# Kernel tuning notes

Hardware: AMD Instinct MI355X
Metric: run time of the kernel (lower is better)

Reference implementation:

```python
import jax, jax.numpy as jnp
import numpy as np

BN_EPS = 1e-5
ATT_EPS = 1e-6


def _conv(x, w, groups=1):
    # x: [B,C,H,W], w: [O, C//groups, k, k], stride 1, SAME padding for odd k
    k = w.shape[-1]
    p = (k - 1) // 2
    return jax.lax.conv_general_dilated(
        x, w, window_strides=(1, 1), padding=[(p, p), (p, p)],
        dimension_numbers=('NCHW', 'OIHW', 'NCHW'), feature_group_count=groups)


def _bn(x, bnp):
    # bnp: [4, C] stacked (scale, bias, running_mean, running_var); eval-mode BN
    s, b, m, v = bnp[0], bnp[1], bnp[2], bnp[3]
    inv = s / jnp.sqrt(v + BN_EPS)
    return x * inv[None, :, None, None] + (b - m * inv)[None, :, None, None]


def _relu6(x):
    return jnp.clip(x, 0.0, 6.0)


def _ffn(x, fc1_w, fc1_bn, conv1_w, conv1_bn, conv2_w, conv2_bn, fc2_w, fc2_bn):
    # E_FFN: 1x1 ConvBNReLU6 -> dw5x5 ConvBNReLU6 & dw3x3 ConvBNReLU6 -> sum -> 1x1 ConvBN -> ReLU6
    C = x.shape[1]
    h = _relu6(_bn(_conv(x, fc1_w), fc1_bn))
    x1 = _relu6(_bn(_conv(h, conv1_w, groups=C), conv1_bn))
    x2 = _relu6(_bn(_conv(h, conv2_w, groups=C), conv2_bn))
    return _relu6(_bn(_conv(x1 + x2, fc2_w), fc2_bn))


def _bias(y, b):
    return y + b[None, :, None, None]


def setup_inputs() -> dict:
    key = jax.random.key(0)
    ks = jax.random.split(key, 16)
    C, M = 64, 8  # in_places, in_places // scale
    B, H, W = 4, 224, 224

    def w(k, shape, s=0.05):
        return (jax.random.normal(k, shape, dtype=jnp.float32) * s)

    def bn_params(k, c):
        k1, k2, k3, k4 = jax.random.split(k, 4)
        scale = 1.0 + 0.1 * jax.random.normal(k1, (c,), dtype=jnp.float32)
        bias = 0.1 * jax.random.normal(k2, (c,), dtype=jnp.float32)
        mean = 0.1 * jax.random.normal(k3, (c,), dtype=jnp.float32)
        var = 1.0 + 0.1 * jax.random.uniform(k4, (c,), dtype=jnp.float32)
        return jnp.stack([scale, bias, mean, var])  # [4, c]

    return {
        'x': jax.random.normal(ks[0], (B, C, H, W), dtype=jnp.float32),
        'gamma': jnp.full((1,), 0.5, dtype=jnp.float32),  # nonzero so attention branch matters
        'q_w': w(ks[1], (M, C, 1, 1)), 'q_b': w(ks[2], (M,)),
        'k_w': w(ks[3], (M, C, 1, 1)), 'k_b': w(ks[4], (M,)),
        'v_w': w(ks[5], (C, C, 1, 1)), 'v_b': w(ks[6], (C,)),
        'fc1_w': w(ks[7], (C, C, 1, 1)), 'fc1_bn': bn_params(ks[8], C),
        'conv1_w': w(ks[9], (C, 1, 5, 5)), 'conv1_bn': bn_params(ks[10], C),
        'conv2_w': w(ks[11], (C, 1, 3, 3)), 'conv2_bn': bn_params(ks[12], C),
        'fc2_w': w(ks[13], (C, C, 1, 1)), 'fc2_bn': bn_params(ks[14], C),
    }


def reference(x, gamma, q_w, q_b, k_w, k_b, v_w, v_b,
              fc1_w, fc1_bn, conv1_w, conv1_bn, conv2_w, conv2_bn, fc2_w, fc2_bn):
    B, C, H, W = x.shape
    N = H * W
    x_channel = _ffn(x, fc1_w, fc1_bn, conv1_w, conv1_bn, conv2_w, conv2_bn, fc2_w, fc2_bn)
    # softplus feature maps; Q,K: [B, m, N]
    Q = jax.nn.softplus(_bias(_conv(x, q_w), q_b).reshape(B, -1, N))
    K = jax.nn.softplus(_bias(_conv(x, k_w), k_b).reshape(B, -1, N))
    V = (_bias(_conv(x, v_w), v_b) + x_channel).reshape(B, C, N)
    Qt = jnp.swapaxes(Q, 1, 2)                              # [B, N, m]
    KV = jnp.einsum('bmn,bcn->bmc', K, V)                   # [B, m, C]
    norm = 1.0 / jnp.einsum('bnm,bm->bn', Qt, K.sum(-1) + ATT_EPS)  # [B, N]
    wv = jnp.einsum('bnm,bmc,bn->bcn', Qt, KV, norm).reshape(B, C, H, W)
    return x + gamma * wv
```

## Files before the change

### kernel.cpp

```cpp
#include <hip/hip_runtime.h>
#include <math.h>

#define B_ 4
#define C_ 64
#define M_ 8
#define H_ 224
#define W_ 224
#define N_ (H_*W_)
#define CN_ (C_*N_)
#define MN_ (M_*N_)
#define BCN_ (B_*CN_)
#define BMN_ (B_*MN_)

__device__ __forceinline__ float relu6f(float v){ return fminf(fmaxf(v,0.0f),6.0f); }
__device__ __forceinline__ float softplusf(float v){
  return v > 0.0f ? v + log1pf(expf(-v)) : log1pf(expf(v));
}

#define FMA4(A, W, X) { A.x = fmaf((W), (X).x, A.x); A.y = fmaf((W), (X).y, A.y); \
                        A.z = fmaf((W), (X).z, A.z); A.w = fmaf((W), (X).w, A.w); }

__global__ __launch_bounds__(256) void k_fc1k(const float* __restrict__ x,
                                              const float* __restrict__ w,
                                              const float* __restrict__ bn,
                                              const float* __restrict__ kw,
                                              const float* __restrict__ kb,
                                              float* __restrict__ h,
                                              float* __restrict__ Kq)
{
  __shared__ float xsl[2*1024];
  __shared__ float wl [2*512];
  __shared__ float kt [512];
  const int tid  = threadIdx.x;
  const int b    = blockIdx.x / 392;
  const int pg   = blockIdx.x % 392;
  const int pix0 = pg*128;
  const float* xb = x + (size_t)b*CN_ + pix0;

  for (int idx = tid; idx < 512; idx += 256) {
    const int c = idx >> 3, m = idx & 7;
    kt[idx] = kw[m*64 + c];
  }

  const int scp = tid >> 5;
  const int spx = (tid & 31) << 2;
  const int e0 = tid*2, e1 = tid*2+1;
  const int wc0 = e0 >> 6, wo0 = e0 & 63;
  const int wc1 = e1 >> 6, wo1 = e1 & 63;

  {
    const float4 xr = *(const float4*)(xb + (size_t)scp*N_ + spx);
    const float w0r = w[wo0*64 + wc0];
    const float w1r = w[wo1*64 + wc1];
    *(float4*)&xsl[scp*128 + spx] = xr;
    wl[e0] = w0r; wl[e1] = w1r;
  }
  __syncthreads();

  const int lane = tid & 63, wv_ = tid >> 6;
  const int och  = 2*wv_ + (lane >> 5);
  const int ocb  = och*8;
  const int px4  = (lane & 31) << 2;

  float4 ah[8];
  float4 ak = {0,0,0,0};
  #pragma unroll
  for (int i = 0; i < 8; ++i) ah[i] = make_float4(0.f,0.f,0.f,0.f);

  for (int ck = 0; ck < 8; ++ck) {
    const int cur = ck & 1, nxt = cur ^ 1;
    const float* xc = &xsl[cur*1024];
    const float* wc = &wl[cur*512];
    float4 xr; float w0r, w1r;
    if (ck < 7) {
      const int c0n = (ck+1)*8;
      xr  = *(const float4*)(xb + (size_t)(c0n + scp)*N_ + spx);
      w0r = w[wo0*64 + c0n + wc0];
      w1r = w[wo1*64 + c0n + wc1];
    }
    #pragma unroll
    for (int cp = 0; cp < 8; ++cp) {
      const float4 xv = *(const float4*)&xc[cp*128 + px4];
      const float4 w0 = *(const float4*)&wc[cp*64 + ocb];
      const float4 w1 = *(const float4*)&wc[cp*64 + ocb + 4];
      const float kvw = kt[(ck*8+cp)*8 + och];
      FMA4(ah[0], w0.x, xv); FMA4(ah[1], w0.y, xv);
      FMA4(ah[2], w0.z, xv); FMA4(ah[3], w0.w, xv);
      FMA4(ah[4], w1.x, xv); FMA4(ah[5], w1.y, xv);
      FMA4(ah[6], w1.z, xv); FMA4(ah[7], w1.w, xv);
      FMA4(ak, kvw, xv);
    }
    if (ck < 7) {
      *(float4*)&xsl[nxt*1024 + scp*128 + spx] = xr;
      wl[nxt*512 + e0] = w0r; wl[nxt*512 + e1] = w1r;
    }
    __syncthreads();
  }

  float* hb = h + (size_t)b*CN_ + pix0 + px4;
  #pragma unroll
  for (int o = 0; o < 8; ++o) {
    const int oc = ocb + o;
    const float inv  = bn[oc] / sqrtf(bn[192+oc] + 1e-5f);
    const float beta = bn[64+oc] - bn[128+oc]*inv;
    float4 o4;
    o4.x = relu6f(fmaf(ah[o].x, inv, beta));
    o4.y = relu6f(fmaf(ah[o].y, inv, beta));
    o4.z = relu6f(fmaf(ah[o].z, inv, beta));
    o4.w = relu6f(fmaf(ah[o].w, inv, beta));
    *(float4*)(hb + (size_t)oc*N_) = o4;
  }
  {
    const float kbm = kb[och];
    float4 q;
    q.x = softplusf(ak.x + kbm); q.y = softplusf(ak.y + kbm);
    q.z = softplusf(ak.z + kbm); q.w = softplusf(ak.w + kbm);
    *(float4*)(Kq + (size_t)b*MN_ + (size_t)och*N_ + pix0 + px4) = q;
  }
}

__global__ __launch_bounds__(256) void k_dw(const float* __restrict__ h,
                                            const float* __restrict__ w5,
                                            const float* __restrict__ w3,
                                            const float* __restrict__ bn1,
                                            const float* __restrict__ bn2,
                                            float* __restrict__ s)
{
  __shared__ float tile[36*37];
  const int tid = threadIdx.x;
  const int blk = blockIdx.x;
  const int t   = blk % 49;
  const int bc  = blk / 49;
  const int c   = bc & 63;
  const int tx0 = (t % 7) * 32;
  const int ty0 = (t / 7) * 32;
  const float* hb = h + (size_t)bc * N_;

  for (int idx = tid; idx < 1296; idx += 256) {
    const int ly = idx / 36, lx = idx - ly*36;
    const int gy = ty0 + ly - 2, gx = tx0 + lx - 2;
    float v = 0.0f;
    if (gy >= 0 && gy < H_ && gx >= 0 && gx < W_) v = hb[gy*W_ + gx];
    tile[ly*37 + lx] = v;
  }
  __syncthreads();

  float w5r[25], w3r[9];
  #pragma unroll
  for (int i = 0; i < 25; ++i) w5r[i] = w5[c*25 + i];
  #pragma unroll
  for (int i = 0; i < 9; ++i)  w3r[i] = w3[c*9 + i];
  const float inv1 = bn1[c] / sqrtf(bn1[192+c] + 1e-5f);
  const float bet1 = bn1[64+c] - bn1[128+c]*inv1;
  const float inv2 = bn2[c] / sqrtf(bn2[192+c] + 1e-5f);
  const float bet2 = bn2[64+c] - bn2[128+c]*inv2;

  const int ty  = tid >> 3;
  const int tx4 = (tid & 7) << 2;
  float a5[4] = {0,0,0,0}, a3[4] = {0,0,0,0};
  #pragma unroll
  for (int dy = 0; dy < 5; ++dy) {
    float r[8];
    #pragma unroll
    for (int i = 0; i < 8; ++i) r[i] = tile[(ty+dy)*37 + tx4 + i];
    #pragma unroll
    for (int dx = 0; dx < 5; ++dx) {
      const float wv = w5r[dy*5+dx];
      #pragma unroll
      for (int p = 0; p < 4; ++p) a5[p] = fmaf(wv, r[p+dx], a5[p]);
    }
    if (dy >= 1 && dy <= 3) {
      #pragma unroll
      for (int dx = 1; dx <= 3; ++dx) {
        const float wv = w3r[(dy-1)*3+(dx-1)];
        #pragma unroll
        for (int p = 0; p < 4; ++p) a3[p] = fmaf(wv, r[p+dx], a3[p]);
      }
    }
  }
  float* sb = s + (size_t)bc * N_ + (ty0+ty)*W_ + tx0 + tx4;
  float4 o4;
  o4.x = relu6f(fmaf(a5[0],inv1,bet1)) + relu6f(fmaf(a3[0],inv2,bet2));
  o4.y = relu6f(fmaf(a5[1],inv1,bet1)) + relu6f(fmaf(a3[1],inv2,bet2));
  o4.z = relu6f(fmaf(a5[2],inv1,bet1)) + relu6f(fmaf(a3[2],inv2,bet2));
  o4.w = relu6f(fmaf(a5[3],inv1,bet1)) + relu6f(fmaf(a3[3],inv2,bet2));
  *(float4*)sb = o4;
}

__global__ __launch_bounds__(256) void k_v(const float* __restrict__ x,
                                           const float* __restrict__ s,
                                           const float* __restrict__ vw,
                                           const float* __restrict__ vb,
                                           const float* __restrict__ fw,
                                           const float* __restrict__ fbn,
                                           float* __restrict__ V)
{
  __shared__ float xsl[2*1024];
  __shared__ float ssl[2*1024];
  __shared__ float wvl[2*512];
  __shared__ float wfl[2*512];
  const int tid  = threadIdx.x;
  const int b    = blockIdx.x / 392;
  const int pg   = blockIdx.x % 392;
  const int pix0 = pg*128;
  const float* xb = x + (size_t)b*CN_ + pix0;
  const float* sb = s + (size_t)b*CN_ + pix0;

  const int scp = tid >> 5;
  const int spx = (tid & 31) << 2;
  const int e0 = tid*2, e1 = tid*2+1;
  const int wc0 = e0 >> 6, wo0 = e0 & 63;
  const int wc1 = e1 >> 6, wo1 = e1 & 63;

  {
    const float4 xr = *(const float4*)(xb + (size_t)scp*N_ + spx);
    const float4 sr = *(const float4*)(sb + (size_t)scp*N_ + spx);
    const float a0 = vw[wo0*64 + wc0], a1 = vw[wo1*64 + wc1];
    const float f0 = fw[wo0*64 + wc0], f1 = fw[wo1*64 + wc1];
    *(float4*)&xsl[scp*128 + spx] = xr;
    *(float4*)&ssl[scp*128 + spx] = sr;
    wvl[e0] = a0; wvl[e1] = a1;
    wfl[e0] = f0; wfl[e1] = f1;
  }
  __syncthreads();

  const int lane = tid & 63, wv_ = tid >> 6;
  const int och  = 2*wv_ + (lane >> 5);
  const int ocb  = och*8;
  const int px4  = (lane & 31) << 2;

  float4 av[8], af[8];
  #pragma unroll
  for (int i = 0; i < 8; ++i) { av[i] = make_float4(0,0,0,0); af[i] = make_float4(0,0,0,0); }

  for (int ck = 0; ck < 8; ++ck) {
    const int cur = ck & 1, nxt = cur ^ 1;
    const float* xc = &xsl[cur*1024];
    const float* sc2 = &ssl[cur*1024];
    const float* wvc = &wvl[cur*512];
    const float* wfc = &wfl[cur*512];
    float4 xr, sr; float a0r, a1r, f0r, f1r;
    if (ck < 7) {
      const int c0n = (ck+1)*8;
      xr  = *(const float4*)(xb + (size_t)(c0n + scp)*N_ + spx);
      sr  = *(const float4*)(sb + (size_t)(c0n + scp)*N_ + spx);
      a0r = vw[wo0*64 + c0n + wc0]; a1r = vw[wo1*64 + c0n + wc1];
      f0r = fw[wo0*64 + c0n + wc0]; f1r = fw[wo1*64 + c0n + wc1];
    }
    #pragma unroll
    for (int cp = 0; cp < 8; ++cp) {
      const float4 xv = *(const float4*)&xc[cp*128 + px4];
      const float4 sv = *(const float4*)&sc2[cp*128 + px4];
      const float4 wa0 = *(const float4*)&wvc[cp*64 + ocb];
      const float4 wa1 = *(const float4*)&wvc[cp*64 + ocb + 4];
      const float4 wf0 = *(const float4*)&wfc[cp*64 + ocb];
      const float4 wf1 = *(const float4*)&wfc[cp*64 + ocb + 4];
      FMA4(av[0], wa0.x, xv); FMA4(av[1], wa0.y, xv);
      FMA4(av[2], wa0.z, xv); FMA4(av[3], wa0.w, xv);
      FMA4(av[4], wa1.x, xv); FMA4(av[5], wa1.y, xv);
      FMA4(av[6], wa1.z, xv); FMA4(av[7], wa1.w, xv);
      FMA4(af[0], wf0.x, sv); FMA4(af[1], wf0.y, sv);
      FMA4(af[2], wf0.z, sv); FMA4(af[3], wf0.w, sv);
      FMA4(af[4], wf1.x, sv); FMA4(af[5], wf1.y, sv);
      FMA4(af[6], wf1.z, sv); FMA4(af[7], wf1.w, sv);
    }
    if (ck < 7) {
      *(float4*)&xsl[nxt*1024 + scp*128 + spx] = xr;
      *(float4*)&ssl[nxt*1024 + scp*128 + spx] = sr;
      wvl[nxt*512 + e0] = a0r; wvl[nxt*512 + e1] = a1r;
      wfl[nxt*512 + e0] = f0r; wfl[nxt*512 + e1] = f1r;
    }
    __syncthreads();
  }

  float* Vb = V + (size_t)b*CN_ + pix0 + px4;
  #pragma unroll
  for (int o = 0; o < 8; ++o) {
    const int oc = ocb + o;
    const float inv  = fbn[oc] / sqrtf(fbn[192+oc] + 1e-5f);
    const float beta = fbn[64+oc] - fbn[128+oc]*inv;
    const float bias = vb[oc];
    float4 o4;
    o4.x = av[o].x + bias + relu6f(fmaf(af[o].x, inv, beta));
    o4.y = av[o].y + bias + relu6f(fmaf(af[o].y, inv, beta));
    o4.z = av[o].z + bias + relu6f(fmaf(af[o].z, inv, beta));
    o4.w = av[o].w + bias + relu6f(fmaf(af[o].w, inv, beta));
    *(float4*)(Vb + (size_t)oc*N_) = o4;
  }
}

__global__ __launch_bounds__(256) void k_kv(const float* __restrict__ V,
                                            const float* __restrict__ Kq,
                                            float* __restrict__ KV,
                                            float* __restrict__ Ksum)
{
  const int blk = blockIdx.x;
  const int b   = blk >> 7;
  const int rem = blk & 127;
  const int cg  = rem >> 4;
  const int ch  = rem & 15;
  const int tid = threadIdx.x;
  const int base = ch * 3136;
  const int end  = base + 3136;
  const float* Kb = Kq + (size_t)b*MN_;
  const float* Vb = V  + (size_t)b*CN_ + (size_t)(cg*8)*N_;

  float acc[64];
  #pragma unroll
  for (int i = 0; i < 64; ++i) acc[i] = 0.0f;
  float ks[8] = {0,0,0,0,0,0,0,0};

  for (int n4 = base + tid*4; n4 < end; n4 += 1024) {
    float4 kr[8];
    #pragma unroll
    for (int m2 = 0; m2 < 8; ++m2) kr[m2] = *(const float4*)(Kb + (size_t)m2*N_ + n4);
    #pragma unroll
    for (int m2 = 0; m2 < 8; ++m2)
      ks[m2] += (kr[m2].x + kr[m2].y) + (kr[m2].z + kr[m2].w);
    #pragma unroll
    for (int c8 = 0; c8 < 8; ++c8) {
      const float4 vv = *(const float4*)(Vb + (size_t)c8*N_ + n4);
      #pragma unroll
      for (int m2 = 0; m2 < 8; ++m2) {
        float t = acc[m2*8+c8];
        t = fmaf(kr[m2].x, vv.x, t);
        t = fmaf(kr[m2].y, vv.y, t);
        t = fmaf(kr[m2].z, vv.z, t);
        t = fmaf(kr[m2].w, vv.w, t);
        acc[m2*8+c8] = t;
      }
    }
  }
  const int lane = tid & 63;

  {
    int nv = 64;
    #pragma unroll
    for (int mask = 1; mask <= 32; mask <<= 1) {
      nv >>= 1;
      const bool hi = (lane & mask) != 0;
      #pragma unroll
      for (int i = 0; i < 32; ++i) {
        if (i < nv) {
          const float mine = hi ? acc[i] : acc[i+nv];
          const float th = __shfl_xor(mine, mask);
          acc[i] = (hi ? acc[i+nv] : acc[i]) + th;
        }
      }
    }
  }
  const int j = 32*(lane & 1) + 16*((lane >> 1) & 1) + 8*((lane >> 2) & 1)
              + 4*((lane >> 3) & 1) + 2*((lane >> 4) & 1) + ((lane >> 5) & 1);
  atomicAdd(&KV[b*512 + (j >> 3)*64 + cg*8 + (j & 7)], acc[0]);

  if (cg == 0) {
    float mk = 0.0f;
    #pragma unroll
    for (int jj = 0; jj < 8; ++jj) {
      float v = ks[jj];
      v += __shfl_xor(v, 1);
      v += __shfl_xor(v, 2);
      v += __shfl_xor(v, 4);
      v += __shfl_xor(v, 8);
      v += __shfl_xor(v, 16);
      v += __shfl_xor(v, 32);
      if (lane == jj) mk = v;
    }
    if (lane < 8) atomicAdd(&Ksum[b*8 + lane], mk);
  }
}

__global__ __launch_bounds__(256) void k_out(const float* __restrict__ x,
                                             const float* __restrict__ qw,
                                             const float* __restrict__ qb,
                                             const float* __restrict__ gamma,
                                             const float* __restrict__ KV,
                                             const float* __restrict__ Ksum,
                                             float* __restrict__ out)
{
  __shared__ __align__(16) float kvt[64*8];
  __shared__ __align__(16) float wqt[64*8];
  __shared__ float ksl[8];
  const int tid = threadIdx.x;
  const int b  = blockIdx.x / 196;
  const int pg = blockIdx.x % 196;
  const int pix0 = pg*256;
  const float* xb = x + (size_t)b*CN_ + pix0 + tid;

  for (int idx = tid; idx < 512; idx += 256) {
    const int m = idx >> 6, c = idx & 63;
    kvt[c*8 + m] = KV[b*512 + idx];
    wqt[c*8 + m] = qw[idx];
  }
  if (tid < 8) ksl[tid] = Ksum[b*8 + tid] + 1e-6f;
  __syncthreads();

  float xr[64];
  float q[8] = {0,0,0,0,0,0,0,0};
  #pragma unroll
  for (int c = 0; c < 64; ++c) {
    xr[c] = xb[(size_t)c*N_];
    const float4 w0 = *(const float4*)&wqt[c*8];
    const float4 w1 = *(const float4*)&wqt[c*8+4];
    q[0] = fmaf(w0.x, xr[c], q[0]);
    q[1] = fmaf(w0.y, xr[c], q[1]);
    q[2] = fmaf(w0.z, xr[c], q[2]);
    q[3] = fmaf(w0.w, xr[c], q[3]);
    q[4] = fmaf(w1.x, xr[c], q[4]);
    q[5] = fmaf(w1.y, xr[c], q[5]);
    q[6] = fmaf(w1.z, xr[c], q[6]);
    q[7] = fmaf(w1.w, xr[c], q[7]);
  }
  float den = 0.0f;
  #pragma unroll
  for (int m = 0; m < 8; ++m) {
    q[m] = softplusf(q[m] + qb[m]);
    den  = fmaf(q[m], ksl[m], den);
  }
  const float sc = gamma[0] / den;

  float* ob = out + (size_t)b*CN_ + pix0 + tid;
  #pragma unroll
  for (int c = 0; c < 64; ++c) {
    const float4 k0 = *(const float4*)&kvt[c*8];
    const float4 k1 = *(const float4*)&kvt[c*8+4];
    float wv;
    wv = q[0]*k0.x;
    wv = fmaf(q[1], k0.y, wv);
    wv = fmaf(q[2], k0.z, wv);
    wv = fmaf(q[3], k0.w, wv);
    wv = fmaf(q[4], k1.x, wv);
    wv = fmaf(q[5], k1.y, wv);
    wv = fmaf(q[6], k1.z, wv);
    wv = fmaf(q[7], k1.w, wv);
    ob[(size_t)c*N_] = fmaf(sc, wv, xr[c]);
  }
}

extern "C" void kernel_launch(void* const* d_in, const int* in_sizes, int n_in,
                              void* d_out, int out_size, void* d_ws, size_t ws_size,
                              hipStream_t stream) {
  const float* x      = (const float*)d_in[0];
  const float* gamma  = (const float*)d_in[1];
  const float* q_w    = (const float*)d_in[2];
  const float* q_b    = (const float*)d_in[3];
  const float* k_w    = (const float*)d_in[4];
  const float* k_b    = (const float*)d_in[5];
  const float* v_w    = (const float*)d_in[6];
  const float* v_b    = (const float*)d_in[7];
  const float* fc1_w  = (const float*)d_in[8];
  const float* fc1_bn = (const float*)d_in[9];
  const float* c1_w   = (const float*)d_in[10];
  const float* c1_bn  = (const float*)d_in[11];
  const float* c2_w   = (const float*)d_in[12];
  const float* c2_bn  = (const float*)d_in[13];
  const float* fc2_w  = (const float*)d_in[14];
  const float* fc2_bn = (const float*)d_in[15];
  float* outp = (float*)d_out;

  float* ws   = (float*)d_ws;
  float* bufA = ws;
  float* bufS = ws + (size_t)BCN_;
  float* bufK = ws + (size_t)2*BCN_;
  float* kv   = ws + (size_t)2*BCN_ + BMN_;
  float* ksum = kv + 2048;

  hipMemsetAsync(kv, 0, (2048 + 32)*sizeof(float), stream);

  k_fc1k<<<dim3(B_*392), dim3(256), 0, stream>>>(x, fc1_w, fc1_bn, k_w, k_b, bufA, bufK);
  k_dw  <<<dim3(B_*C_*49), dim3(256), 0, stream>>>(bufA, c1_w, c2_w, c1_bn, c2_bn, bufS);
  k_v   <<<dim3(B_*392), dim3(256), 0, stream>>>(x, bufS, v_w, v_b, fc2_w, fc2_bn, bufA);
  k_kv  <<<dim3(512), dim3(256), 0, stream>>>(bufA, bufK, kv, ksum);
  k_out <<<dim3(B_*196), dim3(256), 0, stream>>>(x, q_w, q_b, gamma, kv, ksum, outp);
}
```

Before: 347.6 us.

## Compute softplus Q projection inside k_v and read it back in k_out

The 1x1 Q projection and its softplus move into k_v, which already has x staged in shared memory. The result is written into the FFN scratch buffer, which is no longer needed once the block has consumed it. k_out now loads the 8 precomputed Q channels instead of holding 64 channels of x in registers, and re-reads x only for the residual add. This removes k_out's large register array and its Q matmul, which should help occupancy. The cost is extra global writes and reads of the Q buffer.

```diff
diff --git a/kernel.cpp b/kernel.cpp
--- a/kernel.cpp
+++ b/kernel.cpp
@@ -188,23 +188,31 @@
 }
 
 __global__ __launch_bounds__(256) void k_v(const float* __restrict__ x,
-                                           const float* __restrict__ s,
+                                           float* __restrict__ s,
                                            const float* __restrict__ vw,
                                            const float* __restrict__ vb,
                                            const float* __restrict__ fw,
                                            const float* __restrict__ fbn,
+                                           const float* __restrict__ qw_,
+                                           const float* __restrict__ qb_,
                                            float* __restrict__ V)
 {
   __shared__ float xsl[2*1024];
   __shared__ float ssl[2*1024];
   __shared__ float wvl[2*512];
   __shared__ float wfl[2*512];
+  __shared__ float qt [512];
   const int tid  = threadIdx.x;
   const int b    = blockIdx.x / 392;
   const int pg   = blockIdx.x % 392;
   const int pix0 = pg*128;
   const float* xb = x + (size_t)b*CN_ + pix0;
   const float* sb = s + (size_t)b*CN_ + pix0;
+
+  for (int idx = tid; idx < 512; idx += 256) {
+    const int c = idx >> 3, m = idx & 7;
+    qt[idx] = qw_[m*64 + c];
+  }
 
   const int scp = tid >> 5;
   const int spx = (tid & 31) << 2;
@@ -230,6 +238,7 @@
   const int px4  = (lane & 31) << 2;
 
   float4 av[8], af[8];
+  float4 aq = {0,0,0,0};
   #pragma unroll
   for (int i = 0; i < 8; ++i) { av[i] = make_float4(0,0,0,0); af[i] = make_float4(0,0,0,0); }
 
@@ -255,6 +264,7 @@
       const float4 wa1 = *(const float4*)&wvc[cp*64 + ocb + 4];
       const float4 wf0 = *(const float4*)&wfc[cp*64 + ocb];
       const float4 wf1 = *(const float4*)&wfc[cp*64 + ocb + 4];
+      const float qvw = qt[(ck*8+cp)*8 + och];
       FMA4(av[0], wa0.x, xv); FMA4(av[1], wa0.y, xv);
       FMA4(av[2], wa0.z, xv); FMA4(av[3], wa0.w, xv);
       FMA4(av[4], wa1.x, xv); FMA4(av[5], wa1.y, xv);
@@ -263,6 +273,7 @@
       FMA4(af[2], wf0.z, sv); FMA4(af[3], wf0.w, sv);
       FMA4(af[4], wf1.x, sv); FMA4(af[5], wf1.y, sv);
       FMA4(af[6], wf1.z, sv); FMA4(af[7], wf1.w, sv);
+      FMA4(aq, qvw, xv);
     }
     if (ck < 7) {
       *(float4*)&xsl[nxt*1024 + scp*128 + spx] = xr;
@@ -286,6 +297,13 @@
     o4.z = av[o].z + bias + relu6f(fmaf(af[o].z, inv, beta));
     o4.w = av[o].w + bias + relu6f(fmaf(af[o].w, inv, beta));
     *(float4*)(Vb + (size_t)oc*N_) = o4;
+  }
+  {
+    const float qbm = qb_[och];
+    float4 q;
+    q.x = softplusf(aq.x + qbm); q.y = softplusf(aq.y + qbm);
+    q.z = softplusf(aq.z + qbm); q.w = softplusf(aq.w + qbm);
+    *(float4*)(s + (size_t)b*CN_ + (size_t)och*N_ + pix0 + px4) = q;
   }
 }
 
@@ -371,56 +389,38 @@
 }
 
 __global__ __launch_bounds__(256) void k_out(const float* __restrict__ x,
-                                             const float* __restrict__ qw,
-                                             const float* __restrict__ qb,
+                                             const float* __restrict__ Qbuf,
                                              const float* __restrict__ gamma,
                                              const float* __restrict__ KV,
                                              const float* __restrict__ Ksum,
                                              float* __restrict__ out)
 {
   __shared__ __align__(16) float kvt[64*8];
-  __shared__ __align__(16) float wqt[64*8];
   __shared__ float ksl[8];
   const int tid = threadIdx.x;
   const int b  = blockIdx.x / 196;
   const int pg = blockIdx.x % 196;
   const int pix0 = pg*256;
   const float* xb = x + (size_t)b*CN_ + pix0 + tid;
+  const float* Qb = Qbuf + (size_t)b*CN_ + pix0 + tid;
 
   for (int idx = tid; idx < 512; idx += 256) {
     const int m = idx >> 6, c = idx & 63;
     kvt[c*8 + m] = KV[b*512 + idx];
-    wqt[c*8 + m] = qw[idx];
   }
   if (tid < 8) ksl[tid] = Ksum[b*8 + tid] + 1e-6f;
   __syncthreads();
 
-  float xr[64];
-  float q[8] = {0,0,0,0,0,0,0,0};
-  #pragma unroll
-  for (int c = 0; c < 64; ++c) {
-    xr[c] = xb[(size_t)c*N_];
-    const float4 w0 = *(const float4*)&wqt[c*8];
-    const float4 w1 = *(const float4*)&wqt[c*8+4];
-    q[0] = fmaf(w0.x, xr[c], q[0]);
-    q[1] = fmaf(w0.y, xr[c], q[1]);
-    q[2] = fmaf(w0.z, xr[c], q[2]);
-    q[3] = fmaf(w0.w, xr[c], q[3]);
-    q[4] = fmaf(w1.x, xr[c], q[4]);
-    q[5] = fmaf(w1.y, xr[c], q[5]);
-    q[6] = fmaf(w1.z, xr[c], q[6]);
-    q[7] = fmaf(w1.w, xr[c], q[7]);
-  }
+  float q[8];
+  #pragma unroll
+  for (int m = 0; m < 8; ++m) q[m] = Qb[(size_t)m*N_];
   float den = 0.0f;
   #pragma unroll
-  for (int m = 0; m < 8; ++m) {
-    q[m] = softplusf(q[m] + qb[m]);
-    den  = fmaf(q[m], ksl[m], den);
-  }
+  for (int m = 0; m < 8; ++m) den = fmaf(q[m], ksl[m], den);
   const float sc = gamma[0] / den;
 
   float* ob = out + (size_t)b*CN_ + pix0 + tid;
-  #pragma unroll
+  #pragma unroll 8
   for (int c = 0; c < 64; ++c) {
     const float4 k0 = *(const float4*)&kvt[c*8];
     const float4 k1 = *(const float4*)&kvt[c*8+4];
@@ -433,7 +433,7 @@
     wv = fmaf(q[5], k1.y, wv);
     wv = fmaf(q[6], k1.z, wv);
     wv = fmaf(q[7], k1.w, wv);
-    ob[(size_t)c*N_] = fmaf(sc, wv, xr[c]);
+    ob[(size_t)c*N_] = fmaf(sc, wv, xb[(size_t)c*N_]);
   }
 }
 
@@ -469,7 +469,7 @@
 
   k_fc1k<<<dim3(B_*392), dim3(256), 0, stream>>>(x, fc1_w, fc1_bn, k_w, k_b, bufA, bufK);
   k_dw  <<<dim3(B_*C_*49), dim3(256), 0, stream>>>(bufA, c1_w, c2_w, c1_bn, c2_bn, bufS);
-  k_v   <<<dim3(B_*392), dim3(256), 0, stream>>>(x, bufS, v_w, v_b, fc2_w, fc2_bn, bufA);
+  k_v   <<<dim3(B_*392), dim3(256), 0, stream>>>(x, bufS, v_w, v_b, fc2_w, fc2_bn, q_w, q_b, bufA);
   k_kv  <<<dim3(512), dim3(256), 0, stream>>>(bufA, bufK, kv, ksum);
-  k_out <<<dim3(B_*196), dim3(256), 0, stream>>>(x, q_w, q_b, gamma, kv, ksum, outp);
-}
+  k_out <<<dim3(B_*196), dim3(256), 0, stream>>>(x, bufS, gamma, kv, ksum, outp);
+}
```

Result: faster. 300.9 us (-13.4%).

## Stage x tile in shared memory and split k_out work across threads

Applied to the files above, without the earlier changes.

The output kernel now stages a 64-channel by 128-pixel tile of x in shared memory with float4 loads, rather than each thread holding 64 channel values in registers. Half the threads compute the Q projection, softplus and normalisation scale per pixel into shared memory, then all 256 threads cooperatively write the output tile. The grid doubles to cover 128-pixel tiles. This removes the 64-float register array, which should raise occupancy, and vectorises the x reads. The cost is extra synchronisation, 32KB+ of LDS per block, and half the threads sitting idle during the Q phase.

```diff
diff --git a/kernel.cpp b/kernel.cpp
--- a/kernel.cpp
+++ b/kernel.cpp
@@ -378,62 +378,78 @@
                                              const float* __restrict__ Ksum,
                                              float* __restrict__ out)
 {
+  __shared__ float xs[64*128];
   __shared__ __align__(16) float kvt[64*8];
-  __shared__ __align__(16) float wqt[64*8];
+  __shared__ __align__(16) float qwt[64*8];
+  __shared__ float qs[8][128];
+  __shared__ float scl[128];
   __shared__ float ksl[8];
   const int tid = threadIdx.x;
-  const int b  = blockIdx.x / 196;
-  const int pg = blockIdx.x % 196;
-  const int pix0 = pg*256;
-  const float* xb = x + (size_t)b*CN_ + pix0 + tid;
+  const int b  = blockIdx.x / 392;
+  const int pg = blockIdx.x % 392;
+  const int pix0 = pg*128;
+  const float* xb = x + (size_t)b*CN_ + pix0;
 
   for (int idx = tid; idx < 512; idx += 256) {
     const int m = idx >> 6, c = idx & 63;
     kvt[c*8 + m] = KV[b*512 + idx];
-    wqt[c*8 + m] = qw[idx];
+    qwt[c*8 + m] = qw[idx];
   }
   if (tid < 8) ksl[tid] = Ksum[b*8 + tid] + 1e-6f;
+  #pragma unroll
+  for (int i = 0; i < 8; ++i) {
+    const int idx = i*256 + tid;
+    const int c = idx >> 5, p4 = (idx & 31) << 2;
+    const float4 v = *(const float4*)(xb + (size_t)c*N_ + p4);
+    *(float4*)&xs[c*128 + p4] = v;
+  }
   __syncthreads();
 
-  float xr[64];
-  float q[8] = {0,0,0,0,0,0,0,0};
-  #pragma unroll
-  for (int c = 0; c < 64; ++c) {
-    xr[c] = xb[(size_t)c*N_];
-    const float4 w0 = *(const float4*)&wqt[c*8];
-    const float4 w1 = *(const float4*)&wqt[c*8+4];
-    q[0] = fmaf(w0.x, xr[c], q[0]);
-    q[1] = fmaf(w0.y, xr[c], q[1]);
-    q[2] = fmaf(w0.z, xr[c], q[2]);
-    q[3] = fmaf(w0.w, xr[c], q[3]);
-    q[4] = fmaf(w1.x, xr[c], q[4]);
-    q[5] = fmaf(w1.y, xr[c], q[5]);
-    q[6] = fmaf(w1.z, xr[c], q[6]);
-    q[7] = fmaf(w1.w, xr[c], q[7]);
-  }
-  float den = 0.0f;
-  #pragma unroll
-  for (int m = 0; m < 8; ++m) {
-    q[m] = softplusf(q[m] + qb[m]);
-    den  = fmaf(q[m], ksl[m], den);
-  }
-  const float sc = gamma[0] / den;
-
-  float* ob = out + (size_t)b*CN_ + pix0 + tid;
-  #pragma unroll
-  for (int c = 0; c < 64; ++c) {
+  if (tid < 128) {
+    const int px = tid;
+    float q[8] = {0,0,0,0,0,0,0,0};
+    #pragma unroll 8
+    for (int c = 0; c < 64; ++c) {
+      const float xv = xs[c*128 + px];
+      const float4 w0 = *(const float4*)&qwt[c*8];
+      const float4 w1 = *(const float4*)&qwt[c*8+4];
+      q[0] = fmaf(w0.x, xv, q[0]);
+      q[1] = fmaf(w0.y, xv, q[1]);
+      q[2] = fmaf(w0.z, xv, q[2]);
+      q[3] = fmaf(w0.w, xv, q[3]);
+      q[4] = fmaf(w1.x, xv, q[4]);
+      q[5] = fmaf(w1.y, xv, q[5]);
+      q[6] = fmaf(w1.z, xv, q[6]);
+      q[7] = fmaf(w1.w, xv, q[7]);
+    }
+    float den = 0.0f;
+    #pragma unroll
+    for (int m = 0; m < 8; ++m) {
+      q[m] = softplusf(q[m] + qb[m]);
+      den  = fmaf(q[m], ksl[m], den);
+      qs[m][px] = q[m];
+    }
+    scl[px] = gamma[0] / den;
+  }
+  __syncthreads();
+
+  float* ob = out + (size_t)b*CN_ + pix0;
+  #pragma unroll
+  for (int i = 0; i < 32; ++i) {
+    const int idx = i*256 + tid;
+    const int c = idx >> 7, px = idx & 127;
     const float4 k0 = *(const float4*)&kvt[c*8];
     const float4 k1 = *(const float4*)&kvt[c*8+4];
     float wv;
-    wv = q[0]*k0.x;
-    wv = fmaf(q[1], k0.y, wv);
-    wv = fmaf(q[2], k0.z, wv);
-    wv = fmaf(q[3], k0.w, wv);
-    wv = fmaf(q[4], k1.x, wv);
-    wv = fmaf(q[5], k1.y, wv);
-    wv = fmaf(q[6], k1.z, wv);
-    wv = fmaf(q[7], k1.w, wv);
-    ob[(size_t)c*N_] = fmaf(sc, wv, xr[c]);
+    wv = qs[0][px]*k0.x;
+    wv = fmaf(qs[1][px], k0.y, wv);
+    wv = fmaf(qs[2][px], k0.z, wv);
+    wv = fmaf(qs[3][px], k0.w, wv);
+    wv = fmaf(qs[4][px], k1.x, wv);
+    wv = fmaf(qs[5][px], k1.y, wv);
+    wv = fmaf(qs[6][px], k1.z, wv);
+    wv = fmaf(qs[7][px], k1.w, wv);
+    ob[(size_t)c*N_ + px] = fmaf(scl[px], wv, xs[c*128 + px]);
   }
 }
 
@@ -471,5 +487,5 @@
   k_dw  <<<dim3(B_*C_*49), dim3(256), 0, stream>>>(bufA, c1_w, c2_w, c1_bn, c2_bn, bufS);
   k_v   <<<dim3(B_*392), dim3(256), 0, stream>>>(x, bufS, v_w, v_b, fc2_w, fc2_bn, bufA);
   k_kv  <<<dim3(512), dim3(256), 0, stream>>>(bufA, bufK, kv, ksum);
-  k_out <<<dim3(B_*196), dim3(256), 0, stream>>>(x, q_w, q_b, gamma, kv, ksum, outp);
-}
+  k_out <<<dim3(B_*392), dim3(256), 0, stream>>>(x, q_w, q_b, gamma, kv, ksum, outp);
+}
```

Result: faster. 315.2 us (-9.3%).
